# Kernel optimization log

Measured on AMD Instinct MI355X. Metric: run time of the kernel, lower is better.

The kernel has to match this reference:

```python
import jax, jax.numpy as jnp
import numpy as np


def setup_inputs() -> dict:
    key = jax.random.key(0)
    ks = jax.random.split(key, 8)
    B, C, H, W = 4, 256, 64, 64
    QP = 32  # query_planes = inplanes // 8
    x = jax.random.normal(ks[0], (B, C, H, W), dtype=jnp.float32)
    Wq = jax.random.normal(ks[1], (QP, C), dtype=jnp.float32) * (1.0 / np.sqrt(C))
    bq = jax.random.normal(ks[2], (QP,), dtype=jnp.float32) * 0.01
    Wk = jax.random.normal(ks[3], (QP, C), dtype=jnp.float32) * (1.0 / np.sqrt(C))
    bk = jax.random.normal(ks[4], (QP,), dtype=jnp.float32) * 0.01
    Wv = jax.random.normal(ks[5], (C, C), dtype=jnp.float32) * (1.0 / np.sqrt(C))
    bv = jax.random.normal(ks[6], (C,), dtype=jnp.float32) * 0.01
    gamma = jax.random.normal(ks[7], (), dtype=jnp.float32)
    return {"x": x, "Wq": Wq, "bq": bq, "Wk": Wk, "bk": bk,
            "Wv": Wv, "bv": bv, "gamma": gamma}


def reference(x, Wq, bq, Wk, bk, Wv, bv, gamma):
    B, C, H, W = x.shape
    N = H * W
    flat = x.reshape(B, C, N)                              # [B, C, N]
    # 1x1 Conv1d == pointwise linear over channel dim
    q = jnp.einsum('qc,bcn->bnq', Wq, flat) + bq[None, None, :]   # [B, N, QP] (already permuted)
    k = jnp.einsum('qc,bcn->bqn', Wk, flat) + bk[None, :, None]   # [B, QP, N]
    v = jnp.einsum('oc,bcn->bon', Wv, flat) + bv[None, :, None]   # [B, C, N]
    # scores[b, i, j] = <q_i, k_j>, NO 1/sqrt(d) scaling (as in source)
    scores = jnp.einsum('biq,bqj->bij', q, k)              # [B, N, N]
    # unusual softmax axis: dim=1 == over query positions i, per column j
    attn = jax.nn.softmax(scores, axis=1)                  # [B, N, N]
    out_attn = jnp.einsum('bcn,bnj->bcj', v, attn)         # [B, C, N]
    out_attn = out_attn.reshape(B, C, H, W)
    return gamma * out_attn + x
```

## Files before the change

### kernel.cpp

```cpp
#include <hip/hip_runtime.h>
#include <hip/hip_bf16.h>
#include <math.h>


#define NBATCH 4
#define CDIM   256
#define NSEQ   4096
#define QPDIM  32
#define LOG2E  1.44269504088896340736f

typedef _Float16 half8_t  __attribute__((ext_vector_type(8)));
typedef _Float16 half2_t  __attribute__((ext_vector_type(2)));
typedef float    floatx4  __attribute__((ext_vector_type(4)));
typedef float    floatx16 __attribute__((ext_vector_type(16)));

union H8 { half8_t h8; half2_t h2[4]; int i32[4]; };

__device__ inline half2_t pack_f16(float a, float b) {
    return __builtin_bit_cast(half2_t, __builtin_amdgcn_cvt_pkrtz(a, b));
}

__global__ __launch_bounds__(256) void wprep_kernel(
    const float* __restrict__ Wv, const float* __restrict__ Wq,
    const float* __restrict__ Wk, _Float16* __restrict__ wH)
{
    const int idx = blockIdx.x * 256 + threadIdx.x;
    const int e = idx * 8;
    const int r = e >> 8, c = e & 255;
    const float* src;
    float scale = 1.0f;
    if (r < 256)      src = Wv + (size_t)r * 256 + c;
    else if (r < 288) { src = Wq + (size_t)(r - 256) * 256 + c; scale = LOG2E; }
    else              src = Wk + (size_t)(r - 288) * 256 + c;
    float4 f0 = ((const float4*)src)[0];
    float4 f1 = ((const float4*)src)[1];
    half8_t h;
    h[0] = (_Float16)(f0.x * scale); h[1] = (_Float16)(f0.y * scale);
    h[2] = (_Float16)(f0.z * scale); h[3] = (_Float16)(f0.w * scale);
    h[4] = (_Float16)(f1.x * scale); h[5] = (_Float16)(f1.y * scale);
    h[6] = (_Float16)(f1.z * scale); h[7] = (_Float16)(f1.w * scale);
    *(half8_t*)(wH + (size_t)r * 256 + c) = h;
}

__global__ __launch_bounds__(256, 2) void qkv_kernel(
    const float* __restrict__ x, const _Float16* __restrict__ wH,
    const float* __restrict__ bq, const float* __restrict__ bk,
    const float* __restrict__ bv,
    _Float16* __restrict__ qH, _Float16* __restrict__ kH,
    _Float16* __restrict__ vHT)
{
    __shared__ _Float16 xT[64][264];

    const int blk  = blockIdx.x;
    const int slot = blk & 7;
    const int b    = slot >> 1;
    const int n0   = (((blk >> 3) << 1) | (slot & 1)) << 6;
    const int t    = threadIdx.x;
    const int w    = t >> 6;
    const int lane = t & 63;
    const int quad = lane >> 4;
    const int col  = lane & 15;

    {
        const int crow0 = t >> 4;
        const int npart = t & 15;
        #pragma unroll
        for (int pass = 0; pass < 16; ++pass) {
            const int c = pass * 16 + crow0;
            float4 f = *(const float4*)(
                x + ((size_t)(b * CDIM + c)) * NSEQ + n0 + npart * 4);
            xT[npart * 4 + 0][c] = (_Float16)f.x;
            xT[npart * 4 + 1][c] = (_Float16)f.y;
            xT[npart * 4 + 2][c] = (_Float16)f.z;
            xT[npart * 4 + 3][c] = (_Float16)f.w;
        }
    }
    __syncthreads();

    const int r0 = w * 80;
    floatx4 acc[5][4];
    #pragma unroll
    for (int mt = 0; mt < 5; ++mt)
        #pragma unroll
        for (int nt = 0; nt < 4; ++nt)
            acc[mt][nt] = (floatx4){0.f, 0.f, 0.f, 0.f};

    #pragma unroll
    for (int ks = 0; ks < 8; ++ks) {
        half8_t bf[4];
        #pragma unroll
        for (int nt = 0; nt < 4; ++nt)
            bf[nt] = *(const half8_t*)&xT[nt * 16 + col][ks * 32 + quad * 8];
        #pragma unroll
        for (int mt = 0; mt < 5; ++mt) {
            half8_t a = *(const half8_t*)(
                wH + (size_t)(r0 + mt * 16 + col) * 256 + ks * 32 + quad * 8);
            #pragma unroll
            for (int nt = 0; nt < 4; ++nt)
                acc[mt][nt] = __builtin_amdgcn_mfma_f32_16x16x32_f16(
                    a, bf[nt], acc[mt][nt], 0, 0, 0);
        }
    }

    #pragma unroll
    for (int mt = 0; mt < 5; ++mt) {
        const int gbase = r0 + mt * 16;
        const float* bp; int rl; float bscale = 1.0f;
        if (gbase < 256)      { bp = bv; rl = gbase; }
        else if (gbase < 288) { bp = bq; rl = gbase - 256; bscale = LOG2E; }
        else                  { bp = bk; rl = gbase - 288; }
        #pragma unroll
        for (int reg = 0; reg < 4; ++reg) {
            const int rr = rl + quad * 4 + reg;
            const float bias = bp[rr] * bscale;
            #pragma unroll
            for (int nt = 0; nt < 4; ++nt) {
                const int n = n0 + nt * 16 + col;
                const float val = acc[mt][nt][reg] + bias;
                if (gbase < 256)
                    vHT[((size_t)(b * CDIM + rr)) * NSEQ + n] = (_Float16)val;
                else if (gbase < 288)
                    qH[((size_t)(b * NSEQ + n)) * QPDIM + rr] = (_Float16)val;
                else
                    kH[((size_t)(b * NSEQ + n)) * QPDIM + rr] = (_Float16)val;
            }
        }
    }
}

__global__ __launch_bounds__(256, 4) void mpass_kernel(
    const _Float16* __restrict__ qH, const _Float16* __restrict__ kH,
    float* __restrict__ ms4)
{
    __shared__ float wmax[4][32];

    const int blk  = blockIdx.x;
    const int slot = blk & 7;
    const int b    = slot >> 1;
    const int idx  = ((blk >> 3) << 1) | (slot & 1);
    const int jblk = idx & 63;
    const int iq   = idx >> 6;
    const int t    = threadIdx.x;
    const int w    = t >> 6;
    const int lane = t & 63;
    const int l5   = lane >> 5;
    const int lj   = lane & 31;
    const int jt   = w & 1, ih = w >> 1;

    const _Float16* qg = qH + (size_t)b * NSEQ * QPDIM;
    const int j = jblk * 64 + jt * 32 + lj;
    const half8_t kb0 = *(const half8_t*)(
        kH + ((size_t)(b * NSEQ + j)) * QPDIM + l5 * 8);
    const half8_t kb1 = *(const half8_t*)(
        kH + ((size_t)(b * NSEQ + j)) * QPDIM + 16 + l5 * 8);

    float mx = -1e30f;
    const int ibase = iq * 1024 + ih * 512;
    for (int cc = 0; cc < 16; ++cc) {
        const _Float16* qp = qg + (size_t)(ibase + cc * 32 + lj) * QPDIM + l5 * 8;
        half8_t qa0 = *(const half8_t*)qp;
        half8_t qa1 = *(const half8_t*)(qp + 16);
        floatx16 S = __builtin_amdgcn_mfma_f32_32x32x16_f16(
            qa0, kb0, (floatx16){0.f}, 0, 0, 0);
        S = __builtin_amdgcn_mfma_f32_32x32x16_f16(qa1, kb1, S, 0, 0, 0);
        #pragma unroll
        for (int r = 0; r < 16; ++r) mx = fmaxf(mx, S[r]);
    }
    mx = fmaxf(mx, __shfl_xor(mx, 32));
    if (lane < 32) wmax[w][lane] = mx;
    __syncthreads();
    if (t < 64) {
        const int jt3 = t >> 5, c = t & 31;
        ms4[(size_t)iq * (NBATCH * NSEQ) + (size_t)b * NSEQ
            + jblk * 64 + jt3 * 32 + c] = fmaxf(wmax[jt3][c], wmax[jt3 + 2][c]);
    }
}

__global__ __launch_bounds__(256, 2) void attn_kernel(
    const _Float16* __restrict__ qH, const _Float16* __restrict__ kH,
    const _Float16* __restrict__ vHT, const float* __restrict__ ms4,
    const float* __restrict__ x, const float* __restrict__ gamma,
    float* __restrict__ out)
{
    __shared__ _Float16 vbuf[2][8192];
    __shared__ float lred2[2][2][32];

    const int blk  = blockIdx.x;
    const int slot = blk & 7;
    const int b    = slot >> 1;
    const int idx  = ((blk >> 3) << 1) | (slot & 1);
    const int cb   = idx >> 6;
    const int jblk = idx & 63;
    const int j0   = jblk << 6;
    const int c0   = cb << 7;
    const int t    = threadIdx.x;
    const int w    = t >> 6;
    const int lane = t & 63;
    const int l5   = lane >> 5;
    const int lj   = lane & 31;
    const int jh   = w & 1;
    const int ih   = w >> 1;

    const _Float16* qg = qH + (size_t)b * NSEQ * QPDIM;
    const _Float16* vg = vHT + (size_t)b * CDIM * NSEQ;

    const int jme = j0 + jh * 32 + lj;
    const half8_t kb0 = *(const half8_t*)(
        kH + ((size_t)(b * NSEQ + jme)) * QPDIM + l5 * 8);
    const half8_t kb1 = *(const half8_t*)(
        kH + ((size_t)(b * NSEQ + jme)) * QPDIM + 16 + l5 * 8);
    const float* msb = ms4 + (size_t)b * NSEQ + jme;
    const float mfix = fmaxf(
        fmaxf(msb[0], msb[NBATCH * NSEQ]),
        fmaxf(msb[2 * NBATCH * NSEQ], msb[3 * NBATCH * NSEQ]));

    floatx16 acc[4];
    #pragma unroll
    for (int ct = 0; ct < 4; ++ct) acc[ct] = (floatx16){0.f};
    float lp = 0.0f;

    #define DMA_V(i0_, buf_)                                                   \
        {                                                                      \
            _Pragma("unroll")                                                  \
            for (int g = 0; g < 4; ++g) {                                      \
                const int uu = w * 256 + g * 64 + lane;                        \
                const int cl = uu >> 3;                                        \
                const int ck = (uu & 7) ^ (cl & 7);                            \
                const _Float16* src =                                          \
                    vg + (size_t)(c0 + cl) * NSEQ + (i0_) + ck * 8;            \
                __builtin_amdgcn_global_load_lds(                              \
                    (const __attribute__((address_space(1))) void*)src,        \
                    (__attribute__((address_space(3))) void*)                  \
                        (&vbuf[buf_][(w * 256 + g * 64) * 8]),                 \
                    16, 0, 0);                                                 \
            }                                                                  \
        }

    DMA_V(0, 0);
    const _Float16* qb = qg + (size_t)(ih * 32 + lj) * QPDIM + l5 * 8;
    half8_t qa0 = *(const half8_t*)(qb);
    half8_t qa1 = *(const half8_t*)(qb + 16);

    int cur = 0;
    for (int i0 = 0; i0 < NSEQ; i0 += 64) {
        __syncthreads();
        if (i0 + 64 < NSEQ) DMA_V(i0 + 64, cur ^ 1);

        floatx16 S = __builtin_amdgcn_mfma_f32_32x32x16_f16(
            qa0, kb0, (floatx16){0.f}, 0, 0, 0);
        S = __builtin_amdgcn_mfma_f32_32x32x16_f16(qa1, kb1, S, 0, 0, 0);

        H8 lo, hi;
        float ls = 0.0f;
        #pragma unroll
        for (int p = 0; p < 4; ++p) {
            float pa = __builtin_amdgcn_exp2f(S[2 * p]     - mfix);
            float pb = __builtin_amdgcn_exp2f(S[2 * p + 1] - mfix);
            ls += pa + pb;
            lo.h2[p] = pack_f16(pa, pb);
        }
        #pragma unroll
        for (int p = 0; p < 4; ++p) {
            float pa = __builtin_amdgcn_exp2f(S[8 + 2 * p]     - mfix);
            float pb = __builtin_amdgcn_exp2f(S[8 + 2 * p + 1] - mfix);
            ls += pa + pb;
            hi.h2[p] = pack_f16(pa, pb);
        }
        lp += ls;

        H8 shl, shh;
        #pragma unroll
        for (int r = 0; r < 4; ++r) {
            shl.i32[r] = __shfl_xor(lo.i32[r], 32);
            shh.i32[r] = __shfl_xor(hi.i32[r], 32);
        }
        const bool high = (l5 != 0);
        H8 P0, P1;
        P0.i32[0] = high ? shl.i32[2] : lo.i32[0];
        P0.i32[1] = high ? shl.i32[3] : lo.i32[1];
        P0.i32[2] = high ? lo.i32[2]  : shl.i32[0];
        P0.i32[3] = high ? lo.i32[3]  : shl.i32[1];
        P1.i32[0] = high ? shh.i32[2] : hi.i32[0];
        P1.i32[1] = high ? shh.i32[3] : hi.i32[1];
        P1.i32[2] = high ? hi.i32[2]  : shh.i32[0];
        P1.i32[3] = high ? hi.i32[3]  : shh.i32[1];

        #pragma unroll
        for (int ct = 0; ct < 4; ++ct) {
            const int cl = ct * 32 + lj;
            const int ic0 = (ih * 4 + 0 + l5) ^ (cl & 7);
            const int ic1 = (ih * 4 + 2 + l5) ^ (cl & 7);
            half8_t va0 = *(const half8_t*)&vbuf[cur][(cl * 8 + ic0) * 8];
            half8_t va1 = *(const half8_t*)&vbuf[cur][(cl * 8 + ic1) * 8];
            acc[ct] = __builtin_amdgcn_mfma_f32_32x32x16_f16(
                va0, P0.h8, acc[ct], 0, 0, 0);
            acc[ct] = __builtin_amdgcn_mfma_f32_32x32x16_f16(
                va1, P1.h8, acc[ct], 0, 0, 0);
        }

        if (i0 + 64 < NSEQ) {
            qa0 = *(const half8_t*)(qb + (size_t)(i0 + 64) * QPDIM);
            qa1 = *(const half8_t*)(qb + (size_t)(i0 + 64) * QPDIM + 16);
        }
        cur ^= 1;
    }

    lp += __shfl_xor(lp, 32);
    if (lane < 32) lred2[jh][ih][lane] = lp;

    float* fred = (float*)vbuf;
    if (ih == 1) {
        #pragma unroll
        for (int ct = 0; ct < 4; ++ct)
            #pragma unroll
            for (int reg = 0; reg < 16; ++reg) {
                const int crow = (reg & 3) + 8 * (reg >> 2) + 4 * l5;
                fred[(ct * 32 + crow) * 64 + jh * 32 + lj] = acc[ct][reg];
            }
    }
    __syncthreads();

    if (ih == 0) {
        const float rv = gamma[0] / (lred2[jh][0][lj] + lred2[jh][1][lj]);
        #pragma unroll
        for (int ct = 0; ct < 4; ++ct) {
            #pragma unroll
            for (int reg = 0; reg < 16; ++reg) {
                const int crow = (reg & 3) + 8 * (reg >> 2) + 4 * l5;
                const int c_ = c0 + ct * 32 + crow;
                const size_t off = ((size_t)(b * CDIM + c_)) * NSEQ + jme;
                const float sum =
                    acc[ct][reg] + fred[(ct * 32 + crow) * 64 + jh * 32 + lj];
                out[off] = sum * rv + x[off];
            }
        }
    }
}

extern "C" void kernel_launch(void* const* d_in, const int* in_sizes, int n_in,
                              void* d_out, int out_size, void* d_ws, size_t ws_size,
                              hipStream_t stream) {
    const float* x     = (const float*)d_in[0];
    const float* Wq    = (const float*)d_in[1];
    const float* bq    = (const float*)d_in[2];
    const float* Wk    = (const float*)d_in[3];
    const float* bk    = (const float*)d_in[4];
    const float* Wv    = (const float*)d_in[5];
    const float* bv    = (const float*)d_in[6];
    const float* gamma = (const float*)d_in[7];
    float* out = (float*)d_out;

    _Float16* w16 = (_Float16*)d_ws;
    _Float16* qH  = w16;
    _Float16* kH  = qH + (size_t)NBATCH * NSEQ * QPDIM;
    _Float16* vHT = kH + (size_t)NBATCH * NSEQ * QPDIM;
    _Float16* wH  = vHT + (size_t)NBATCH * CDIM * NSEQ;
    float*    ms4 = (float*)(wH + (size_t)320 * 256);

    wprep_kernel<<<40, 256, 0, stream>>>(Wv, Wq, Wk, wH);
    qkv_kernel<<<256, 256, 0, stream>>>(x, wH, bq, bk, bv, qH, kH, vHT);
    mpass_kernel<<<1024, 256, 0, stream>>>(qH, kH, ms4);
    attn_kernel<<<512, 256, 0, stream>>>(qH, kH, vHT, ms4, x, gamma, out);
}
```

Baseline: 184.1 us.

## Software-pipeline PV MFMA one step behind softmax with triple-buffered V; halve QKV tiles

```diff
diff --git a/kernel.cpp b/kernel.cpp
--- a/kernel.cpp
+++ b/kernel.cpp
@@ -42,19 +42,19 @@
     *(half8_t*)(wH + (size_t)r * 256 + c) = h;
 }
 
-__global__ __launch_bounds__(256, 2) void qkv_kernel(
+__global__ __launch_bounds__(256, 4) void qkv_kernel(
     const float* __restrict__ x, const _Float16* __restrict__ wH,
     const float* __restrict__ bq, const float* __restrict__ bk,
     const float* __restrict__ bv,
     _Float16* __restrict__ qH, _Float16* __restrict__ kH,
     _Float16* __restrict__ vHT)
 {
-    __shared__ _Float16 xT[64][264];
+    __shared__ _Float16 xT[32][264];
 
     const int blk  = blockIdx.x;
     const int slot = blk & 7;
     const int b    = slot >> 1;
-    const int n0   = (((blk >> 3) << 1) | (slot & 1)) << 6;
+    const int n0   = (((blk >> 3) << 1) | (slot & 1)) << 5;
     const int t    = threadIdx.x;
     const int w    = t >> 6;
     const int lane = t & 63;
@@ -62,43 +62,40 @@
     const int col  = lane & 15;
 
     {
-        const int crow0 = t >> 4;
-        const int npart = t & 15;
-        #pragma unroll
-        for (int pass = 0; pass < 16; ++pass) {
-            const int c = pass * 16 + crow0;
+        const int crow = t >> 3;
+        const int np   = t & 7;
+        #pragma unroll
+        for (int pass = 0; pass < 8; ++pass) {
+            const int c = pass * 32 + crow;
             float4 f = *(const float4*)(
-                x + ((size_t)(b * CDIM + c)) * NSEQ + n0 + npart * 4);
-            xT[npart * 4 + 0][c] = (_Float16)f.x;
-            xT[npart * 4 + 1][c] = (_Float16)f.y;
-            xT[npart * 4 + 2][c] = (_Float16)f.z;
-            xT[npart * 4 + 3][c] = (_Float16)f.w;
+                x + ((size_t)(b * CDIM + c)) * NSEQ + n0 + np * 4);
+            xT[np * 4 + 0][c] = (_Float16)f.x;
+            xT[np * 4 + 1][c] = (_Float16)f.y;
+            xT[np * 4 + 2][c] = (_Float16)f.z;
+            xT[np * 4 + 3][c] = (_Float16)f.w;
         }
     }
     __syncthreads();
 
     const int r0 = w * 80;
-    floatx4 acc[5][4];
-    #pragma unroll
-    for (int mt = 0; mt < 5; ++mt)
-        #pragma unroll
-        for (int nt = 0; nt < 4; ++nt)
-            acc[mt][nt] = (floatx4){0.f, 0.f, 0.f, 0.f};
-
+    floatx4 acc[5][2];
+    #pragma unroll
+    for (int mt = 0; mt < 5; ++mt) {
+        acc[mt][0] = (floatx4){0.f, 0.f, 0.f, 0.f};
+        acc[mt][1] = (floatx4){0.f, 0.f, 0.f, 0.f};
+    }
     #pragma unroll
     for (int ks = 0; ks < 8; ++ks) {
-        half8_t bf[4];
-        #pragma unroll
-        for (int nt = 0; nt < 4; ++nt)
-            bf[nt] = *(const half8_t*)&xT[nt * 16 + col][ks * 32 + quad * 8];
+        half8_t bf0 = *(const half8_t*)&xT[col][ks * 32 + quad * 8];
+        half8_t bf1 = *(const half8_t*)&xT[16 + col][ks * 32 + quad * 8];
         #pragma unroll
         for (int mt = 0; mt < 5; ++mt) {
             half8_t a = *(const half8_t*)(
                 wH + (size_t)(r0 + mt * 16 + col) * 256 + ks * 32 + quad * 8);
-            #pragma unroll
-            for (int nt = 0; nt < 4; ++nt)
-                acc[mt][nt] = __builtin_amdgcn_mfma_f32_16x16x32_f16(
-                    a, bf[nt], acc[mt][nt], 0, 0, 0);
+            acc[mt][0] = __builtin_amdgcn_mfma_f32_16x16x32_f16(
+                a, bf0, acc[mt][0], 0, 0, 0);
+            acc[mt][1] = __builtin_amdgcn_mfma_f32_16x16x32_f16(
+                a, bf1, acc[mt][1], 0, 0, 0);
         }
     }
 
@@ -114,7 +111,7 @@
             const int rr = rl + quad * 4 + reg;
             const float bias = bp[rr] * bscale;
             #pragma unroll
-            for (int nt = 0; nt < 4; ++nt) {
+            for (int nt = 0; nt < 2; ++nt) {
                 const int n = n0 + nt * 16 + col;
                 const float val = acc[mt][nt][reg] + bias;
                 if (gbase < 256)
@@ -182,7 +179,7 @@
     const float* __restrict__ x, const float* __restrict__ gamma,
     float* __restrict__ out)
 {
-    __shared__ _Float16 vbuf[2][8192];
+    __shared__ _Float16 vbuf[3][8192];
     __shared__ float lred2[2][2][32];
 
     const int blk  = blockIdx.x;
@@ -214,6 +211,10 @@
         fmaxf(msb[0], msb[NBATCH * NSEQ]),
         fmaxf(msb[2 * NBATCH * NSEQ], msb[3 * NBATCH * NSEQ]));
 
+    floatx16 cinit;
+    #pragma unroll
+    for (int r = 0; r < 16; ++r) cinit[r] = -mfix;
+
     floatx16 acc[4];
     #pragma unroll
     for (int ct = 0; ct < 4; ++ct) acc[ct] = (floatx16){0.f};
@@ -241,28 +242,46 @@
     half8_t qa0 = *(const half8_t*)(qb);
     half8_t qa1 = *(const half8_t*)(qb + 16);
 
-    int cur = 0;
+    H8 P0p, P1p;
+    int bread = 0, bdma = 1, bpv = 2;
+
     for (int i0 = 0; i0 < NSEQ; i0 += 64) {
         __syncthreads();
-        if (i0 + 64 < NSEQ) DMA_V(i0 + 64, cur ^ 1);
+
+        if (i0 + 64 < NSEQ) DMA_V(i0 + 64, bdma);
 
         floatx16 S = __builtin_amdgcn_mfma_f32_32x32x16_f16(
-            qa0, kb0, (floatx16){0.f}, 0, 0, 0);
+            qa0, kb0, cinit, 0, 0, 0);
         S = __builtin_amdgcn_mfma_f32_32x32x16_f16(qa1, kb1, S, 0, 0, 0);
+
+        if (i0 != 0) {
+            #pragma unroll
+            for (int ct = 0; ct < 4; ++ct) {
+                const int cl = ct * 32 + lj;
+                const int ic0 = (ih * 4 + 0 + l5) ^ (cl & 7);
+                const int ic1 = (ih * 4 + 2 + l5) ^ (cl & 7);
+                half8_t va0 = *(const half8_t*)&vbuf[bpv][(cl * 8 + ic0) * 8];
+                half8_t va1 = *(const half8_t*)&vbuf[bpv][(cl * 8 + ic1) * 8];
+                acc[ct] = __builtin_amdgcn_mfma_f32_32x32x16_f16(
+                    va0, P0p.h8, acc[ct], 0, 0, 0);
+                acc[ct] = __builtin_amdgcn_mfma_f32_32x32x16_f16(
+                    va1, P1p.h8, acc[ct], 0, 0, 0);
+            }
+        }
 
         H8 lo, hi;
         float ls = 0.0f;
         #pragma unroll
         for (int p = 0; p < 4; ++p) {
-            float pa = __builtin_amdgcn_exp2f(S[2 * p]     - mfix);
-            float pb = __builtin_amdgcn_exp2f(S[2 * p + 1] - mfix);
+            float pa = __builtin_amdgcn_exp2f(S[2 * p]);
+            float pb = __builtin_amdgcn_exp2f(S[2 * p + 1]);
             ls += pa + pb;
             lo.h2[p] = pack_f16(pa, pb);
         }
         #pragma unroll
         for (int p = 0; p < 4; ++p) {
-            float pa = __builtin_amdgcn_exp2f(S[8 + 2 * p]     - mfix);
-            float pb = __builtin_amdgcn_exp2f(S[8 + 2 * p + 1] - mfix);
+            float pa = __builtin_amdgcn_exp2f(S[8 + 2 * p]);
+            float pb = __builtin_amdgcn_exp2f(S[8 + 2 * p + 1]);
             ls += pa + pb;
             hi.h2[p] = pack_f16(pa, pb);
         }
@@ -275,38 +294,39 @@
             shh.i32[r] = __shfl_xor(hi.i32[r], 32);
         }
         const bool high = (l5 != 0);
-        H8 P0, P1;
-        P0.i32[0] = high ? shl.i32[2] : lo.i32[0];
-        P0.i32[1] = high ? shl.i32[3] : lo.i32[1];
-        P0.i32[2] = high ? lo.i32[2]  : shl.i32[0];
-        P0.i32[3] = high ? lo.i32[3]  : shl.i32[1];
-        P1.i32[0] = high ? shh.i32[2] : hi.i32[0];
-        P1.i32[1] = high ? shh.i32[3] : hi.i32[1];
-        P1.i32[2] = high ? hi.i32[2]  : shh.i32[0];
-        P1.i32[3] = high ? hi.i32[3]  : shh.i32[1];
-
-        #pragma unroll
-        for (int ct = 0; ct < 4; ++ct) {
-            const int cl = ct * 32 + lj;
-            const int ic0 = (ih * 4 + 0 + l5) ^ (cl & 7);
-            const int ic1 = (ih * 4 + 2 + l5) ^ (cl & 7);
-            half8_t va0 = *(const half8_t*)&vbuf[cur][(cl * 8 + ic0) * 8];
-            half8_t va1 = *(const half8_t*)&vbuf[cur][(cl * 8 + ic1) * 8];
-            acc[ct] = __builtin_amdgcn_mfma_f32_32x32x16_f16(
-                va0, P0.h8, acc[ct], 0, 0, 0);
-            acc[ct] = __builtin_amdgcn_mfma_f32_32x32x16_f16(
-                va1, P1.h8, acc[ct], 0, 0, 0);
-        }
+        P0p.i32[0] = high ? shl.i32[2] : lo.i32[0];
+        P0p.i32[1] = high ? shl.i32[3] : lo.i32[1];
+        P0p.i32[2] = high ? lo.i32[2]  : shl.i32[0];
+        P0p.i32[3] = high ? lo.i32[3]  : shl.i32[1];
+        P1p.i32[0] = high ? shh.i32[2] : hi.i32[0];
+        P1p.i32[1] = high ? shh.i32[3] : hi.i32[1];
+        P1p.i32[2] = high ? hi.i32[2]  : shh.i32[0];
+        P1p.i32[3] = high ? hi.i32[3]  : shh.i32[1];
 
         if (i0 + 64 < NSEQ) {
             qa0 = *(const half8_t*)(qb + (size_t)(i0 + 64) * QPDIM);
             qa1 = *(const half8_t*)(qb + (size_t)(i0 + 64) * QPDIM + 16);
         }
-        cur ^= 1;
+
+        int tmp = bread; bread = bdma; bdma = bpv; bpv = tmp;
+    }
+
+    #pragma unroll
+    for (int ct = 0; ct < 4; ++ct) {
+        const int cl = ct * 32 + lj;
+        const int ic0 = (ih * 4 + 0 + l5) ^ (cl & 7);
+        const int ic1 = (ih * 4 + 2 + l5) ^ (cl & 7);
+        half8_t va0 = *(const half8_t*)&vbuf[bpv][(cl * 8 + ic0) * 8];
+        half8_t va1 = *(const half8_t*)&vbuf[bpv][(cl * 8 + ic1) * 8];
+        acc[ct] = __builtin_amdgcn_mfma_f32_32x32x16_f16(
+            va0, P0p.h8, acc[ct], 0, 0, 0);
+        acc[ct] = __builtin_amdgcn_mfma_f32_32x32x16_f16(
+            va1, P1p.h8, acc[ct], 0, 0, 0);
     }
 
     lp += __shfl_xor(lp, 32);
     if (lane < 32) lred2[jh][ih][lane] = lp;
+    __syncthreads();
 
     float* fred = (float*)vbuf;
     if (ih == 1) {
@@ -358,7 +378,7 @@
     float*    ms4 = (float*)(wH + (size_t)320 * 256);
 
     wprep_kernel<<<40, 256, 0, stream>>>(Wv, Wq, Wk, wH);
-    qkv_kernel<<<256, 256, 0, stream>>>(x, wH, bq, bk, bv, qH, kH, vHT);
+    qkv_kernel<<<512, 256, 0, stream>>>(x, wH, bq, bk, bv, qH, kH, vHT);
     mpass_kernel<<<1024, 256, 0, stream>>>(qH, kH, ms4);
     attn_kernel<<<512, 256, 0, stream>>>(qH, kH, vHT, ms4, x, gamma, out);
 }
```

New measurement: 187.8 us. Within noise of the previous version (+2.0%).
